# Performance work log

Measured on AMD Instinct MI355X. Metric: run time of the kernel, lower is better.

Reference implementation:

```python
import jax, jax.numpy as jnp
import numpy as np

NUM_EMB = 8192
EMB_DIM = 64
TOP_K = 10
TEMP = 1.0
PERP_W = 0.01


def setup_inputs() -> dict:
    key = jax.random.key(0)
    k1, k2, k3 = jax.random.split(key, 3)
    inputs = jax.random.normal(k1, (8, 2048, EMB_DIM), dtype=jnp.float32)
    codebook = jax.random.normal(k2, (NUM_EMB, EMB_DIM), dtype=jnp.float32)
    # Gumbel noise for vectorized multinomial sampling over top-k (Gumbel-max trick)
    u = jax.random.uniform(k3, (8 * 2048, TOP_K), dtype=jnp.float32, minval=1e-6, maxval=1.0 - 1e-6)
    gumbel = -jnp.log(-jnp.log(u))
    return {"inputs": inputs, "codebook": codebook, "gumbel": gumbel}


def _vq_forward(inputs, codebook, gumbel):
    K, D = codebook.shape
    shp = inputs.shape
    flat = inputs.reshape(-1, D)                      # [N, D]
    valid = jnp.linalg.norm(flat, axis=1) > 1e-6      # [N]
    d = (jnp.sum(flat * flat, axis=1, keepdims=True)
         + jnp.sum(codebook * codebook, axis=1)
         - 2.0 * (flat @ codebook.T))
    # top-k smallest distances
    neg_top, top_idx = jax.lax.top_k(-d, TOP_K)       # [N, k]
    top_d = -neg_top
    logits = -top_d / TEMP
    # multinomial(softmax(logits)) sample per row via Gumbel-max (vectorized)
    j = jnp.argmax(logits + gumbel, axis=1)           # [N]
    rows = jnp.arange(flat.shape[0])
    idx = top_idx[rows, j]                            # sampled codebook indices [N]
    min_d = top_d[rows, j]                            # sampled distances [N]
    q_valid = codebook[idx]                           # embedding gather [N, D]
    vmask = valid[:, None].astype(flat.dtype)
    q_flat = q_valid * vmask                          # zero rows where invalid
    idx_flat = jnp.where(valid, idx, 0)
    min_d_flat = jnp.where(valid, min_d, jnp.zeros((), flat.dtype))
    n_valid = jnp.maximum(jnp.sum(valid.astype(flat.dtype)), 1.0)
    # codebook (VQ) loss: MSE over valid rows; commitment loss has 0 weight in source
    loss_vq = jnp.sum(vmask * (q_valid - jax.lax.stop_gradient(flat)) ** 2) / (n_valid * D)
    quantized = q_flat.reshape(shp)
    quantized_st = inputs + jax.lax.stop_gradient(quantized - inputs)
    # usage / perplexity from one-hot scatter-add over valid rows
    counts = jnp.zeros(K, dtype=flat.dtype).at[idx].add(valid.astype(flat.dtype))
    avg_probs = counts / n_valid
    perplexity = jnp.exp(-jnp.sum(avg_probs * jnp.log(avg_probs + 1e-10)))
    perplexity_loss = -jnp.log(perplexity + 1e-10)
    total_loss = loss_vq + PERP_W * perplexity_loss
    return quantized_st, total_loss, idx_flat, min_d_flat, perplexity


def reference(inputs, codebook, gumbel):
    return _vq_forward(inputs, codebook, gumbel)
```

## Files before the change

kernel.cpp:

```cpp
#include <hip/hip_runtime.h>
#include <hip/hip_bf16.h>

#define N_ROWS   16384
#define EMB_DIM  64
#define NUM_EMB  8192
#define TOP_K    10
#define PERP_W   0.01


#define QST_OFF   0
#define LOSS_OFF  (N_ROWS * EMB_DIM)
#define IDX_OFF   (LOSS_OFF + 1)
#define MIND_OFF  (IDX_OFF + N_ROWS)
#define PERP_OFF  (MIND_OFF + N_ROWS)

#define WS_E2C    0
#define WS_E2D    32768
#define WS_CBS    98304
#define WS_HIST   1146880
#define WS_LOSSP  1179648
#define WS_NVP    1212416
#define WS_C32    1228800

typedef short bf16x8 __attribute__((ext_vector_type(8)));
typedef float f32x4  __attribute__((ext_vector_type(4)));

__device__ __forceinline__ unsigned umx(unsigned a, unsigned b) {
    return __builtin_elementwise_max(a, b);
}
__device__ __forceinline__ unsigned umn(unsigned a, unsigned b) {
    return __builtin_elementwise_min(a, b);
}

__device__ __forceinline__ unsigned short f2bf(float f) {
    unsigned int u = __float_as_uint(f);
    unsigned int r = u + 0x7fffu + ((u >> 16) & 1u);
    return (unsigned short)(r >> 16);
}

__global__ __launch_bounds__(256) void vq_prep(const float* __restrict__ cb,
                                               float* __restrict__ e2c,
                                               double* __restrict__ e2d,
                                               unsigned short* __restrict__ cbs,
                                               int* __restrict__ hist) {
    const int g  = blockIdx.x * 256 + threadIdx.x;
    const int k  = g >> 2;
    const int lq = g & 3;

    if (g < NUM_EMB) hist[g] = 0;

    const float4* rp = (const float4*)(cb + (size_t)k * EMB_DIM + lq * 16);
    float  s  = 0.0f;
    double sd = 0.0;
    unsigned pk[8];
#pragma unroll
    for (int i = 0; i < 4; ++i) {
        const float4 v = rp[i];
        s  += v.x * v.x + v.y * v.y + v.z * v.z + v.w * v.w;
        sd += (double)v.x * (double)v.x + (double)v.y * (double)v.y
            + (double)v.z * (double)v.z + (double)v.w * (double)v.w;
        pk[2 * i + 0] = (unsigned)f2bf(v.x) | ((unsigned)f2bf(v.y) << 16);
        pk[2 * i + 1] = (unsigned)f2bf(v.z) | ((unsigned)f2bf(v.w) << 16);
    }
    s  += __shfl_xor(s, 1);  s  += __shfl_xor(s, 2);
    sd += __shfl_xor(sd, 1); sd += __shfl_xor(sd, 2);
    if (lq == 0) { e2c[k] = 512.0f - 0.5f * s; e2d[k] = sd; }

    const int tp = k >> 5, r32 = k & 31, rsub = r32 & 15;
    unsigned short* basep = cbs + ((size_t)tp << 11)
                          + ((unsigned)(r32 & 16) << 6)
                          + (rsub << 3);
    const int hi  = lq >> 1;
    const int q2s = (lq & 1) * 2;
    uint4 c0, c1;
    c0.x = pk[0]; c0.y = pk[1]; c0.z = pk[2]; c0.w = pk[3];
    c1.x = pk[4]; c1.y = pk[5]; c1.z = pk[6]; c1.w = pk[7];
    *(uint4*)(basep + hi * 512 + (q2s + 0) * 128) = c0;
    *(uint4*)(basep + hi * 512 + (q2s + 1) * 128) = c1;
}

__global__ __launch_bounds__(256) void vq_gemm_topk(
        const float* __restrict__ inp, const unsigned short* __restrict__ cbs,
        const float* __restrict__ e2c, unsigned short* __restrict__ cand32) {
    __shared__ unsigned keysh[16][193];

    const int tid   = threadIdx.x;
    const int w     = tid >> 6;
    const int lane  = tid & 63;
    const int q     = lane >> 4;
    const int rsub  = lane & 15;
    const int row0  = blockIdx.x * 16;
    const int row   = row0 + rsub;
    const int half0 = blockIdx.y * 4096;
    const int cbase = half0 + w * 1024;
    const int tpbase = cbase >> 5;

    const int eoff = q << 2;

    bf16x8 b0, b1;
    {
        const float* xp = inp + (size_t)row * EMB_DIM + q * 8;
#pragma unroll
        for (int j = 0; j < 8; ++j) b0[j] = (short)f2bf(xp[j]);
#pragma unroll
        for (int j = 0; j < 8; ++j) b1[j] = (short)f2bf(xp[32 + j]);
    }

    unsigned la[12], lb[12];
#pragma unroll
    for (int i = 0; i < 12; ++i) { la[i] = 0u; lb[i] = 0u; }

#define LOADP(P0,P1,P2,P3,E0,E1,TT) { \
        const bf16x8* bp_ = ((const bf16x8*)cbs) + (size_t)(tpbase + (TT)) * 256; \
        P0 = bp_[lane];        P1 = bp_[lane + 64]; \
        P2 = bp_[lane + 128];  P3 = bp_[lane + 192]; \
        const float* ep_ = e2c + cbase + (TT) * 32; \
        E0 = *(const f32x4*)(ep_ + eoff); \
        E1 = *(const f32x4*)(ep_ + eoff + 16); }

    bf16x8 A00, A01, A10, A11, B00, B01, B10, B11;
    f32x4  Ae0, Ae1, Be0, Be1;
    LOADP(A00, A01, A10, A11, Ae0, Ae1, 0)
    LOADP(B00, B01, B10, B11, Be0, Be1, 1)

#define CE(A,B) { const unsigned mx_ = umx(A, B), mn_ = umn(A, B); \
                  A = mx_; B = mn_; }

#define SORT3(A,B,C) { const unsigned x3_ = A, y3_ = B, z3_ = C; \
        unsigned mx3_, md3_, mn3_; \
        asm("v_max3_u32 %0, %1, %2, %3" : "=v"(mx3_) : "v"(x3_), "v"(y3_), "v"(z3_)); \
        asm("v_med3_u32 %0, %1, %2, %3" : "=v"(md3_) : "v"(x3_), "v"(y3_), "v"(z3_)); \
        asm("v_min3_u32 %0, %1, %2, %3" : "=v"(mn3_) : "v"(x3_), "v"(y3_), "v"(z3_)); \
        A = mx3_; B = md3_; C = mn3_; }

#define RESORT(L) { \
        CE(L[0],L[6]) CE(L[1],L[7]) CE(L[2],L[8])  CE(L[3],L[9])  CE(L[4],L[10]) CE(L[5],L[11]) \
        CE(L[0],L[3]) CE(L[1],L[4]) CE(L[2],L[5])  CE(L[6],L[9])  CE(L[7],L[10]) CE(L[8],L[11]) \
        SORT3(L[0],L[1],L[2]) SORT3(L[3],L[4],L[5]) \
        SORT3(L[6],L[7],L[8]) SORT3(L[9],L[10],L[11]) }

#define SUBITER(P0,P1,P2,P3,E0,E1,TT,TP,L) { \
        const bf16x8 c00_ = P0, c01_ = P1, c10_ = P2, c11_ = P3; \
        const f32x4  ce0_ = E0, ce1_ = E1; \
        LOADP(P0, P1, P2, P3, E0, E1, (TP) & 31) \
        f32x4 acc0_ = __builtin_amdgcn_mfma_f32_16x16x32_bf16(c00_, b0, ce0_, 0, 0, 0); \
        acc0_       = __builtin_amdgcn_mfma_f32_16x16x32_bf16(c01_, b1, acc0_, 0, 0, 0); \
        f32x4 acc1_ = __builtin_amdgcn_mfma_f32_16x16x32_bf16(c10_, b0, ce1_, 0, 0, 0); \
        acc1_       = __builtin_amdgcn_mfma_f32_16x16x32_bf16(c11_, b1, acc1_, 0, 0, 0); \
        const unsigned tb_ = (unsigned)((TT) << 3); \
        unsigned k0 = (__float_as_uint(acc0_[0]) & 0xFFFFFF00u) | (tb_ + 0u); \
        unsigned k1 = (__float_as_uint(acc0_[1]) & 0xFFFFFF00u) | (tb_ + 1u); \
        unsigned k2 = (__float_as_uint(acc0_[2]) & 0xFFFFFF00u) | (tb_ + 2u); \
        unsigned k3 = (__float_as_uint(acc0_[3]) & 0xFFFFFF00u) | (tb_ + 3u); \
        unsigned k4 = (__float_as_uint(acc1_[0]) & 0xFFFFFF00u) | (tb_ + 4u); \
        unsigned k5 = (__float_as_uint(acc1_[1]) & 0xFFFFFF00u) | (tb_ + 5u); \
        unsigned k6 = (__float_as_uint(acc1_[2]) & 0xFFFFFF00u) | (tb_ + 6u); \
        unsigned k7 = (__float_as_uint(acc1_[3]) & 0xFFFFFF00u) | (tb_ + 7u); \
         \
        CE(k0,k1) CE(k2,k3) CE(k4,k5) CE(k6,k7) \
        CE(k0,k2) CE(k1,k3) CE(k4,k6) CE(k5,k7) \
        CE(k1,k2) CE(k5,k6) \
        CE(k0,k4) CE(k1,k5) CE(k2,k6) CE(k3,k7) \
        CE(k2,k4) CE(k3,k5) \
        CE(k1,k2) CE(k3,k4) CE(k5,k6) \
         \
        CE(L[11],k0) CE(L[10],k1) CE(L[9],k2) CE(L[8],k3) \
        CE(L[7],k4)  CE(L[6],k5)  CE(L[5],k6) CE(L[4],k7) \
        RESORT(L) }

    for (int t = 0; t < 32; t += 2) {
        SUBITER(A00, A01, A10, A11, Ae0, Ae1, t,     t + 2, la)
        SUBITER(B00, B01, B10, B11, Be0, Be1, t + 1, t + 3, lb)
    }
#undef SUBITER
#undef LOADP

    CE(la[11], lb[0]) CE(la[10], lb[1]) CE(la[9], lb[2])  CE(la[8], lb[3])
    CE(la[7],  lb[4]) CE(la[6],  lb[5]) CE(la[5], lb[6])  CE(la[4], lb[7])
    CE(la[3],  lb[8]) CE(la[2],  lb[9]) CE(la[1], lb[10]) CE(la[0], lb[11])
    RESORT(la)
#undef RESORT
#undef SORT3
#undef CE

    {
        unsigned* kr = &keysh[rsub][w * 48 + q * 12];
#pragma unroll
        for (int i = 0; i < 12; ++i) kr[i] = la[i];
    }
    __syncthreads();

    for (int rr = 0; rr < 4; ++rr) {
        const int lr = 4 * w + rr;
        const unsigned ka = keysh[lr][lane];
        const unsigned kb = keysh[lr][lane + 64];
        const unsigned kc = keysh[lr][lane + 128];

        unsigned tau = 0u;
#pragma unroll
        for (int b = 31; b >= 0; --b) {
            const unsigned t2 = tau | (1u << b);
            const int cnt = __popcll(__ballot(ka >= t2))
                          + __popcll(__ballot(kb >= t2))
                          + __popcll(__ballot(kc >= t2));
            if (cnt >= 16) tau = t2;
        }

        const unsigned long long m0 = __ballot(ka >= tau);
        const unsigned long long m1 = __ballot(kb >= tau);
        const unsigned long long m2 = __ballot(kc >= tau);
        const unsigned long long below = (lane == 0) ? 0ull
                                        : (~0ull >> (64 - lane));
        const int c0 = __popcll(m0);
        const int c1 = __popcll(m1);
        const int p0 = __popcll(m0 & below);
        const int p1 = c0 + __popcll(m1 & below);
        const int p2 = c0 + c1 + __popcll(m2 & below);

        unsigned short* outp =
            cand32 + (size_t)(row0 + lr) * 32 + blockIdx.y * 16;

#define EMIT(KX, SLOT, POS) \
        if ((KX) >= tau && (POS) < 16) { \
            const unsigned slot_ = (unsigned)(SLOT); \
            const unsigned idx_  = (KX) & 0xFFu; \
            const unsigned wq_   = slot_ / 48u; \
            const unsigned qq_   = (slot_ % 48u) / 12u; \
            const unsigned code_ = (unsigned)half0 + wq_ * 1024u \
                                 + ((idx_ >> 3) << 5) + (((idx_ >> 2) & 1u) << 4) \
                                 + (qq_ << 2) + (idx_ & 3u); \
            outp[POS] = (unsigned short)code_; \
        }
        EMIT(ka, lane,       p0)
        EMIT(kb, lane + 64,  p1)
        EMIT(kc, lane + 128, p2)
#undef EMIT
    }
}

__global__ __launch_bounds__(256) void vq_finalize(const float* __restrict__ inp,
                                                   const float* __restrict__ cb,
                                                   const double* __restrict__ e2d,
                                                   const float* __restrict__ gumbel,
                                                   const unsigned short* __restrict__ cand32,
                                                   float* __restrict__ out,
                                                   int* __restrict__ hist,
                                                   double* __restrict__ lossp,
                                                   int* __restrict__ nvp) {
    __shared__ double dvs[4][32];
    __shared__ int    dis[4][32];
    __shared__ double wl[4];
    __shared__ int    wv[4];

    const int tid  = threadIdx.x;
    const int w    = tid >> 6;
    const int lane = tid & 63;
    const int row  = blockIdx.x * 4 + w;
    const int g    = lane >> 2;
    const int lq   = lane & 3;

    const float xf = inp[(size_t)row * EMB_DIM + lane];
    const double xd = (double)xf;

    const int code0 = (int)cand32[(size_t)row * 32 + g];
    const int code1 = (int)cand32[(size_t)row * 32 + 16 + g];
    const float4* ep0 = (const float4*)(cb + ((size_t)code0 << 6) + (lq << 4));
    const float4* ep1 = (const float4*)(cb + ((size_t)code1 << 6) + (lq << 4));
    const float4 a0 = ep0[0], a1 = ep0[1], a2 = ep0[2], a3 = ep0[3];
    const float4 b0 = ep1[0], b1 = ep1[1], b2 = ep1[2], b3 = ep1[3];
    const double ed0 = e2d[code0];
    const double ed1 = e2d[code1];

    double x2 = xd * xd;
#pragma unroll
    for (int off = 32; off >= 1; off >>= 1) x2 += __shfl_xor(x2, off);
    const bool valid = x2 > 1e-12;

    const float4* xp = (const float4*)(inp + (size_t)row * EMB_DIM + (lq << 4));
    const float4 xv0 = xp[0], xv1 = xp[1], xv2 = xp[2], xv3 = xp[3];

#define DOT16(V0,V1,V2,V3, EDV, J, CODE) { \
        double d0_ = 0.0, d1_ = 0.0; \
        d0_ = fma((double)xv0.x, (double)V0.x, d0_);  d0_ = fma((double)xv0.y, (double)V0.y, d0_); \
        d0_ = fma((double)xv0.z, (double)V0.z, d0_);  d0_ = fma((double)xv0.w, (double)V0.w, d0_); \
        d0_ = fma((double)xv1.x, (double)V1.x, d0_);  d0_ = fma((double)xv1.y, (double)V1.y, d0_); \
        d0_ = fma((double)xv1.z, (double)V1.z, d0_);  d0_ = fma((double)xv1.w, (double)V1.w, d0_); \
        d1_ = fma((double)xv2.x, (double)V2.x, d1_);  d1_ = fma((double)xv2.y, (double)V2.y, d1_); \
        d1_ = fma((double)xv2.z, (double)V2.z, d1_);  d1_ = fma((double)xv2.w, (double)V2.w, d1_); \
        d1_ = fma((double)xv3.x, (double)V3.x, d1_);  d1_ = fma((double)xv3.y, (double)V3.y, d1_); \
        d1_ = fma((double)xv3.z, (double)V3.z, d1_);  d1_ = fma((double)xv3.w, (double)V3.w, d1_); \
        double dot_ = d0_ + d1_; \
        dot_ += __shfl_xor(dot_, 1); \
        dot_ += __shfl_xor(dot_, 2); \
        if (lq == 0) { \
            dvs[w][J] = x2 + (EDV) - 2.0 * dot_; \
            dis[w][J] = (CODE); \
        } }

    DOT16(a0, a1, a2, a3, ed0, g,      code0)
    DOT16(b0, b1, b2, b3, ed1, 16 + g, code1)
#undef DOT16
    __syncthreads();

    const bool has = (lane < 32);
    double cd = has ? dvs[w][lane] : 1.0e300;
    int    ci = has ? dis[w][lane] : 0x7fffffff;

    int rank = 0;
#pragma unroll
    for (int off = 1; off < 32; ++off) {
        const double od = __shfl_xor(cd, off);
        const int    oi = __shfl_xor(ci, off);
        if (od < cd || (od == cd && oi < ci)) ++rank;
    }

    float sc = -3.0e38f;
    if (has && rank < TOP_K)
        sc = (float)(-cd) + gumbel[(size_t)row * TOP_K + rank];

    double bd = cd; int bi = ci; int brk = rank;
#pragma unroll
    for (int off = 1; off < 64; off <<= 1) {
        const float  os = __shfl_xor(sc, off);
        const double od = __shfl_xor(bd, off);
        const int    oi = __shfl_xor(bi, off);
        const int    ork = __shfl_xor(brk, off);
        if (os > sc || (os == sc && ork < brk)) {
            sc = os; bd = od; bi = oi; brk = ork;
        }
    }
    const int   cidx = bi;
    const float mind = (float)bd;

    const float vm = valid ? 1.0f : 0.0f;
    const float qv = cb[(size_t)cidx * EMB_DIM + lane];
    out[QST_OFF + (size_t)row * EMB_DIM + lane] = xf + (qv * vm - xf);

    const double dq = (double)qv - xd;
    double l = dq * dq * (double)vm;
#pragma unroll
    for (int off = 32; off >= 1; off >>= 1) l += __shfl_xor(l, off);

    if (lane == 0) {
        wl[w] = l;
        wv[w] = valid ? 1 : 0;
        if (valid) atomicAdd(&hist[cidx], 1);
        out[IDX_OFF + row]  = valid ? (float)cidx : 0.0f;
        out[MIND_OFF + row] = valid ? mind : 0.0f;
    }
    __syncthreads();
    if (tid == 0) {
        lossp[blockIdx.x] = wl[0] + wl[1] + wl[2] + wl[3];
        nvp[blockIdx.x]   = wv[0] + wv[1] + wv[2] + wv[3];
    }
}

__global__ __launch_bounds__(1024) void vq_entropy(const int* __restrict__ nvp,
                                                   const int* __restrict__ hist,
                                                   double* __restrict__ hpart) {
    __shared__ int    redi[1024];
    __shared__ double red[1024];
    const int tid = threadIdx.x;

    int nvl = 0;
#pragma unroll
    for (int i = 0; i < 4; ++i) nvl += nvp[tid + 1024 * i];
    redi[tid] = nvl;
    __syncthreads();
    for (int s = 512; s >= 1; s >>= 1) {
        if (tid < s) redi[tid] += redi[tid + s];
        __syncthreads();
    }
    const double nv = (redi[0] > 0) ? (double)redi[0] : 1.0;

    const int k = blockIdx.x * 1024 + tid;
    const double p = (double)hist[k] / nv;
    red[tid] = p * log(p + 1e-10);
    __syncthreads();
    for (int s = 512; s >= 1; s >>= 1) {
        if (tid < s) red[tid] += red[tid + s];
        __syncthreads();
    }
    if (tid == 0) hpart[blockIdx.x] = red[0];
}

__global__ __launch_bounds__(1024) void vq_scalars(const double* __restrict__ lossp,
                                                   const int* __restrict__ nvp,
                                                   const double* __restrict__ hpart,
                                                   float* __restrict__ out) {
    __shared__ double red[1024];
    __shared__ double s_nv;
    const int tid = threadIdx.x;

    double lsum = 0.0;
    int    nvl  = 0;
#pragma unroll
    for (int i = 0; i < 4; ++i) {
        const int j = tid + 1024 * i;
        lsum += lossp[j];
        nvl  += nvp[j];
    }

    red[tid] = lsum;
    __syncthreads();
    for (int s = 512; s >= 1; s >>= 1) {
        if (tid < s) red[tid] += red[tid + s];
        __syncthreads();
    }
    const double losstot = red[0];
    __syncthreads();

    red[tid] = (double)nvl;
    __syncthreads();
    for (int s = 512; s >= 1; s >>= 1) {
        if (tid < s) red[tid] += red[tid + s];
        __syncthreads();
    }
    if (tid == 0) s_nv = (red[0] > 0.5) ? red[0] : 1.0;
    __syncthreads();
    const double nv = s_nv;

    if (tid == 0) {
        double H = 0.0;
#pragma unroll
        for (int b = 0; b < 8; ++b) H += hpart[b];
        const double perp = exp(-H);
        const double ploss = -log(perp + 1e-10);
        const double lvq = losstot / (nv * (double)EMB_DIM);
        out[LOSS_OFF] = (float)(lvq + PERP_W * ploss);
        out[PERP_OFF] = (float)perp;
    }
}

extern "C" void kernel_launch(void* const* d_in, const int* in_sizes, int n_in,
                              void* d_out, int out_size, void* d_ws, size_t ws_size,
                              hipStream_t stream) {
    const float* inp    = (const float*)d_in[0];
    const float* cb     = (const float*)d_in[1];
    const float* gumbel = (const float*)d_in[2];
    float* out = (float*)d_out;

    char* ws = (char*)d_ws;
    float*          e2c    = (float*)(ws + WS_E2C);
    double*         e2d    = (double*)(ws + WS_E2D);
    unsigned short* cbs    = (unsigned short*)(ws + WS_CBS);
    int*            hist   = (int*)(ws + WS_HIST);
    double*         lossp  = (double*)(ws + WS_LOSSP);
    int*            nvp    = (int*)(ws + WS_NVP);
    unsigned short* cand32 = (unsigned short*)(ws + WS_C32);
    double*         hpart  = (double*)(ws + WS_C32);

    vq_prep<<<NUM_EMB * 4 / 256, 256, 0, stream>>>(cb, e2c, e2d, cbs, hist);
    vq_gemm_topk<<<dim3(N_ROWS / 16, 2), 256, 0, stream>>>(inp, cbs, e2c, cand32);
    vq_finalize<<<N_ROWS / 4, 256, 0, stream>>>(inp, cb, e2d, gumbel, cand32, out,
                                                hist, lossp, nvp);
    vq_entropy<<<8, 1024, 0, stream>>>(nvp, hist, hpart);
    vq_scalars<<<1, 1024, 0, stream>>>(lossp, nvp, hpart, out);
}
```

Before: 175.4 us.

## Stream codebook tiles into LDS via async global_load_lds double buffering

Replaces per-lane register prefetch of codebook tiles and e2c values with direct global-to-LDS async loads, double-buffered per wave with explicit vmcnt waits. The per-wave e2c slice is preloaded into LDS once. The intent is to free VGPRs and overlap memory latency with the MFMA and sort work. It adds LDS traffic, a larger shared footprint that may lower occupancy, and relies on hand-tuned waitcnt ordering. The keysh scratch array now aliases the same shared buffer, with a barrier added before it is reused.

```diff
diff --git a/kernel.cpp b/kernel.cpp
--- a/kernel.cpp
+++ b/kernel.cpp
@@ -36,6 +36,17 @@
     unsigned int u = __float_as_uint(f);
     unsigned int r = u + 0x7fffu + ((u >> 16) & 1u);
     return (unsigned short)(r >> 16);
+}
+
+__device__ __forceinline__ void gll16(const void* g, void* l) {
+    __builtin_amdgcn_global_load_lds(
+        (const __attribute__((address_space(1))) unsigned int*)g,
+        (__attribute__((address_space(3))) unsigned int*)l, 16, 0, 0);
+}
+__device__ __forceinline__ void gll4(const void* g, void* l) {
+    __builtin_amdgcn_global_load_lds(
+        (const __attribute__((address_space(1))) unsigned int*)g,
+        (__attribute__((address_space(3))) unsigned int*)l, 4, 0, 0);
 }
 
 __global__ __launch_bounds__(256) void vq_prep(const float* __restrict__ cb,
@@ -79,10 +90,13 @@
     *(uint4*)(basep + hi * 512 + (q2s + 1) * 128) = c1;
 }
 
+#define E2C_REGION 16384
+#define TBUF_BYTES 4096
+
 __global__ __launch_bounds__(256) void vq_gemm_topk(
         const float* __restrict__ inp, const unsigned short* __restrict__ cbs,
         const float* __restrict__ e2c, unsigned short* __restrict__ cand32) {
-    __shared__ unsigned keysh[16][193];
+    __shared__ __align__(16) char smem[E2C_REGION + 4 * 2 * TBUF_BYTES];
 
     const int tid   = threadIdx.x;
     const int w     = tid >> 6;
@@ -97,6 +111,27 @@
 
     const int eoff = q << 2;
 
+    char* e2cb = smem + w * 4096;
+    char* tbuf = smem + E2C_REGION + w * 2 * TBUF_BYTES;
+    const char* gt = (const char*)cbs + ((size_t)tpbase << 12) + (size_t)lane * 16;
+
+#define GLL_TILE(BUFI, TT) { \
+        const char* g_ = gt + ((size_t)(TT) << 12); \
+        char* l_ = tbuf + (BUFI) * TBUF_BYTES; \
+        gll16(g_,        l_); \
+        gll16(g_ + 1024, l_ + 1024); \
+        gll16(g_ + 2048, l_ + 2048); \
+        gll16(g_ + 3072, l_ + 3072); }
+
+    {
+        const float* ge = e2c + cbase + lane;
+#pragma unroll
+        for (int j = 0; j < 16; ++j)
+            gll4(ge + j * 64, e2cb + j * 256);
+    }
+    GLL_TILE(0, 0)
+    GLL_TILE(1, 1)
+
     bf16x8 b0, b1;
     {
         const float* xp = inp + (size_t)row * EMB_DIM + q * 8;
@@ -109,19 +144,6 @@
     unsigned la[12], lb[12];
 #pragma unroll
     for (int i = 0; i < 12; ++i) { la[i] = 0u; lb[i] = 0u; }
-
-#define LOADP(P0,P1,P2,P3,E0,E1,TT) { \
-        const bf16x8* bp_ = ((const bf16x8*)cbs) + (size_t)(tpbase + (TT)) * 256; \
-        P0 = bp_[lane];        P1 = bp_[lane + 64]; \
-        P2 = bp_[lane + 128];  P3 = bp_[lane + 192]; \
-        const float* ep_ = e2c + cbase + (TT) * 32; \
-        E0 = *(const f32x4*)(ep_ + eoff); \
-        E1 = *(const f32x4*)(ep_ + eoff + 16); }
-
-    bf16x8 A00, A01, A10, A11, B00, B01, B10, B11;
-    f32x4  Ae0, Ae1, Be0, Be1;
-    LOADP(A00, A01, A10, A11, Ae0, Ae1, 0)
-    LOADP(B00, B01, B10, B11, Be0, Be1, 1)
 
 #define CE(A,B) { const unsigned mx_ = umx(A, B), mn_ = umn(A, B); \
                   A = mx_; B = mn_; }
@@ -139,10 +161,16 @@
         SORT3(L[0],L[1],L[2]) SORT3(L[3],L[4],L[5]) \
         SORT3(L[6],L[7],L[8]) SORT3(L[9],L[10],L[11]) }
 
-#define SUBITER(P0,P1,P2,P3,E0,E1,TT,TP,L) { \
-        const bf16x8 c00_ = P0, c01_ = P1, c10_ = P2, c11_ = P3; \
-        const f32x4  ce0_ = E0, ce1_ = E1; \
-        LOADP(P0, P1, P2, P3, E0, E1, (TP) & 31) \
+#define SUBITER(TT, BUFI, L) { \
+        asm volatile("s_waitcnt vmcnt(4)" ::: "memory"); \
+        __builtin_amdgcn_sched_barrier(0); \
+        const char* cbuf_ = tbuf + (BUFI) * TBUF_BYTES; \
+        const bf16x8* lp_ = (const bf16x8*)cbuf_; \
+        const bf16x8 c00_ = lp_[lane],        c01_ = lp_[lane + 64]; \
+        const bf16x8 c10_ = lp_[lane + 128],  c11_ = lp_[lane + 192]; \
+        const float* le_ = (const float*)(e2cb + (TT) * 128); \
+        const f32x4 ce0_ = *(const f32x4*)(le_ + eoff); \
+        const f32x4 ce1_ = *(const f32x4*)(le_ + eoff + 16); \
         f32x4 acc0_ = __builtin_amdgcn_mfma_f32_16x16x32_bf16(c00_, b0, ce0_, 0, 0, 0); \
         acc0_       = __builtin_amdgcn_mfma_f32_16x16x32_bf16(c01_, b1, acc0_, 0, 0, 0); \
         f32x4 acc1_ = __builtin_amdgcn_mfma_f32_16x16x32_bf16(c10_, b0, ce1_, 0, 0, 0); \
@@ -166,14 +194,16 @@
          \
         CE(L[11],k0) CE(L[10],k1) CE(L[9],k2) CE(L[8],k3) \
         CE(L[7],k4)  CE(L[6],k5)  CE(L[5],k6) CE(L[4],k7) \
-        RESORT(L) }
+        RESORT(L) \
+        __builtin_amdgcn_sched_barrier(0); \
+        GLL_TILE(BUFI, ((TT) + 2) & 31) }
 
     for (int t = 0; t < 32; t += 2) {
-        SUBITER(A00, A01, A10, A11, Ae0, Ae1, t,     t + 2, la)
-        SUBITER(B00, B01, B10, B11, Be0, Be1, t + 1, t + 3, lb)
+        SUBITER(t,     0, la)
+        SUBITER(t + 1, 1, lb)
     }
 #undef SUBITER
-#undef LOADP
+#undef GLL_TILE
 
     CE(la[11], lb[0]) CE(la[10], lb[1]) CE(la[9], lb[2])  CE(la[8], lb[3])
     CE(la[7],  lb[4]) CE(la[6],  lb[5]) CE(la[5], lb[6])  CE(la[4], lb[7])
@@ -182,6 +212,9 @@
 #undef RESORT
 #undef SORT3
 #undef CE
+
+    unsigned (*keysh)[193] = reinterpret_cast<unsigned(*)[193]>(smem);
+    __syncthreads();
 
     {
         unsigned* kr = &keysh[rsub][w * 48 + q * 12];
```

Result: slower. 180.3 us (+2.8%).
